# Optimization experiments

Hardware: AMD Instinct MI355X
Metric: run time of the kernel (lower is better)

## Reference

```python
import jax, jax.numpy as jnp
import numpy as np

B, L, D = 2, 2048, 1024
NUM_HEADS = 16
HEAD_DIM = D // NUM_HEADS


def setup_inputs() -> dict:
    key = jax.random.key(0)
    k1, k2 = jax.random.split(key)
    x = jax.random.normal(k1, (B, L, D), dtype=jnp.float32)
    # torch Linear(input_dim, 3*output_dim, bias=False); store as [in, 3*out] for x @ W
    W_qkv = jax.random.normal(k2, (D, 3 * D), dtype=jnp.float32) * (1.0 / np.sqrt(D))
    return {"x": x, "W_qkv": W_qkv}


def reference(x, W_qkv):
    b, l, d = x.shape
    h, hd = NUM_HEADS, HEAD_DIM
    qkv = x @ W_qkv                                  # [B, L, 3*D]
    qkv = qkv.reshape(b, l, 3, h, hd)
    q = jnp.transpose(qkv[:, :, 0], (0, 2, 1, 3))    # [B, H, L, hd]
    k = jnp.transpose(qkv[:, :, 1], (0, 2, 1, 3))
    v = jnp.transpose(qkv[:, :, 2], (0, 2, 1, 3))
    scale = 1.0 / jnp.sqrt(jnp.asarray(hd, dtype=x.dtype))
    scores = jnp.einsum('bhqd,bhkd->bhqk', q, k) * scale   # [B, H, L, L]
    causal = jnp.triu(jnp.ones((l, l), dtype=bool), k=1)   # True above diagonal -> masked
    scores = jnp.where(causal, -jnp.inf, scores)
    attn = jax.nn.softmax(scores, axis=-1)
    # dropout p=0.0 -> identity (eval mode)
    out = jnp.einsum('bhqk,bhkd->bhqd', attn, v)            # [B, H, L, hd]
    out = jnp.transpose(out, (0, 2, 1, 3)).reshape(b, l, h * hd)
    return out
```

## Files before the change

### kernel.cpp

```cpp
#include <hip/hip_runtime.h>
#include <hip/hip_bf16.h>
#include <math.h>

#define NB_L 2048
#define GM 4096
#define GN 3072
#define GK 1024
#define NROWS 65536
#define SCALE_L2E 0.180336880f

typedef float  f4v __attribute__((ext_vector_type(4)));
typedef short  s4v __attribute__((ext_vector_type(4)));
typedef short  s8v __attribute__((ext_vector_type(8)));

#define MFMA_16x16x32(a, b, c) __builtin_amdgcn_mfma_f32_16x16x32_bf16((a), (b), (c), 0, 0, 0)
#define MFMA_16x16x16(a, b, c) __builtin_amdgcn_mfma_f32_16x16x16bf16_1k((a), (b), (c), 0, 0, 0)

static __device__ __forceinline__ unsigned int bfpk(float a, float b) {
    __hip_bfloat162 h = __float22bfloat162_rn(float2{a, b});
    union { __hip_bfloat162 h2; unsigned int u; } cv; cv.h2 = h; return cv.u;
}
static __device__ __forceinline__ unsigned int pkrnd(float a, float b) {
    union { float f; unsigned int u; } ua, ub;
    ua.f = a; ub.f = b;
    return __builtin_amdgcn_perm(ub.u + 0x8000u, ua.u + 0x8000u, 0x07060302u);
}
static __device__ __forceinline__ unsigned short bf1(float a) {
    union { __hip_bfloat16 h; unsigned short u; } cv; cv.h = __float2bfloat16(a); return cv.u;
}
static __device__ __forceinline__ float bf2f(unsigned short u) {
    union { unsigned int u; float f; } cv; cv.u = ((unsigned int)u) << 16; return cv.f;
}

static __device__ __forceinline__ void gl_lds16(const ushort* g, ushort* l) {
    __builtin_amdgcn_global_load_lds((const __attribute__((address_space(1))) void*)g,
                                     (__attribute__((address_space(3))) void*)l, 16, 0, 0);
}

__global__ __launch_bounds__(256) void conv_fused(
    const float* __restrict__ X, const float* __restrict__ W,
    ushort* __restrict__ Xb, ushort* __restrict__ Wt)
{
    __shared__ __align__(16) ushort T[64][72];
    const int bid = blockIdx.x, t = threadIdx.x;
    if (bid < 2048) {
        const int i = bid * 256 + t;
        const float4 f0 = ((const float4*)X)[2 * i];
        const float4 f1 = ((const float4*)X)[2 * i + 1];
        uint4 u;
        u.x = bfpk(f0.x, f0.y); u.y = bfpk(f0.z, f0.w);
        u.z = bfpk(f1.x, f1.y); u.w = bfpk(f1.z, f1.w);
        ((uint4*)Xb)[i] = u;
    } else {
        const int wb = bid - 2048;
        const int k0 = (wb & 15) * 64, n0 = (wb >> 4) * 64;
        {
            const int kr = t >> 2, nc0 = (t & 3) * 16;
            const float* src = W + (size_t)(k0 + kr) * GN + n0 + nc0;
#pragma unroll
            for (int u = 0; u < 4; ++u) {
                const float4 v = *(const float4*)(src + 4 * u);
                T[nc0 + 4 * u + 0][kr] = bf1(v.x);
                T[nc0 + 4 * u + 1][kr] = bf1(v.y);
                T[nc0 + 4 * u + 2][kr] = bf1(v.z);
                T[nc0 + 4 * u + 3][kr] = bf1(v.w);
            }
        }
        __syncthreads();
        {
            const int nr = t >> 2, kc0 = (t & 3) * 16;
            ushort* dst = Wt + (size_t)(n0 + nr) * GK + k0 + kc0;
            *(s8v*)dst       = *(const s8v*)&T[nr][kc0];
            *(s8v*)(dst + 8) = *(const s8v*)&T[nr][kc0 + 8];
        }
    }
}

__global__ __launch_bounds__(512, 2) void qkv_gemm_bf16(
    const ushort* __restrict__ Xb, const ushort* __restrict__ Wt,
    ushort* __restrict__ Qh, ushort* __restrict__ Kh, ushort* __restrict__ VT)
{
    __shared__ __align__(16) ushort As[2][2][128][32];
    __shared__ __align__(16) ushort Bs[2][2][384][32];

    const int tid = threadIdx.x;
    const int bid = blockIdx.x;

    const int xcd = bid & 7, idx = bid >> 3;
    const int ytile = ((xcd >> 1) << 3) + (idx & 7);
    const int xtile = ((xcd & 1) << 2) + (idx >> 3);
    const int row0 = ytile << 7;
    const int col0 = xtile * 384;

    const int lane = tid & 63, w = tid >> 6;
    const int wm = w >> 2, wn = w & 3;
    const int lq = lane & 15, quad = lane >> 4;

    const int rS = tid >> 2, pA = tid & 3;
    const int cA = pA ^ ((rS >> 1) & 3);
    const ushort* gA0 = Xb + (size_t)(row0 + rS) * GK + cA * 8;
    const ushort* gB0 = Wt + (size_t)(col0 + rS) * GK + cA * 8;

    const int pq = (quad ^ ((lq >> 1) & 3)) * 8;
    const int rowA = wm * 64 + lq;
    const int rowB = wn * 96 + lq;

    f4v acc[4][6];
#pragma unroll
    for (int mf = 0; mf < 4; ++mf)
#pragma unroll
        for (int nf = 0; nf < 6; ++nf) acc[mf][nf] = 0.f;

    auto stA = [&](int t, int h) {
        gl_lds16(gA0 + t * 64 + h * 32, &As[t & 1][h][rS][pA * 8]);
    };
    auto stB = [&](int t, int h, int u) {
        gl_lds16(gB0 + (size_t)u * 128 * GK + t * 64 + h * 32,
                 &Bs[t & 1][h][u * 128 + rS][pA * 8]);
    };

    stA(0, 0);
    stB(0, 0, 0); stB(0, 0, 1); stB(0, 0, 2);
    stA(0, 1);
    stB(0, 1, 0); stB(0, 1, 1); stB(0, 1, 2);
    stA(1, 0);
    stB(1, 0, 0); stB(1, 0, 1); stB(1, 0, 2);
    asm volatile("s_waitcnt vmcnt(4)" ::: "memory");
    __builtin_amdgcn_s_barrier();
    asm volatile("" ::: "memory");

    const int NT = GK / 64;
#pragma unroll 2
    for (int t = 0; t < NT; ++t) {
        const int cur = t & 1;
        s8v af[4], bfr[3];

#pragma unroll
        for (int nf = 0; nf < 3; ++nf) bfr[nf] = *(const s8v*)&Bs[cur][0][rowB + nf * 16][pq];
#pragma unroll
        for (int mf = 0; mf < 4; ++mf) af[mf] = *(const s8v*)&As[cur][0][rowA + mf * 16][pq];
        if (t + 1 < NT) { stB(t + 1, 1, 0); stB(t + 1, 1, 1); stB(t + 1, 1, 2); }
        __builtin_amdgcn_s_barrier();
        asm volatile("s_waitcnt lgkmcnt(0)");
        __builtin_amdgcn_s_setprio(1);
#pragma unroll
        for (int mf = 0; mf < 4; ++mf)
#pragma unroll
            for (int nf = 0; nf < 3; ++nf)
                acc[mf][nf] = MFMA_16x16x32(af[mf], bfr[nf], acc[mf][nf]);
        __builtin_amdgcn_s_setprio(0);
        __builtin_amdgcn_s_barrier();

#pragma unroll
        for (int nf = 0; nf < 3; ++nf) bfr[nf] = *(const s8v*)&Bs[cur][0][rowB + 48 + nf * 16][pq];
        if (t + 1 < NT) stA(t + 1, 1);
        __builtin_amdgcn_s_barrier();
        asm volatile("s_waitcnt lgkmcnt(0)");
        __builtin_amdgcn_s_setprio(1);
#pragma unroll
        for (int mf = 0; mf < 4; ++mf)
#pragma unroll
            for (int nf = 0; nf < 3; ++nf)
                acc[mf][nf + 3] = MFMA_16x16x32(af[mf], bfr[nf], acc[mf][nf + 3]);
        __builtin_amdgcn_s_setprio(0);
        __builtin_amdgcn_s_barrier();

#pragma unroll
        for (int nf = 0; nf < 3; ++nf) bfr[nf] = *(const s8v*)&Bs[cur][1][rowB + nf * 16][pq];
#pragma unroll
        for (int mf = 0; mf < 4; ++mf) af[mf] = *(const s8v*)&As[cur][1][rowA + mf * 16][pq];
        if (t + 2 < NT) stA(t + 2, 0);
        __builtin_amdgcn_s_barrier();
        asm volatile("s_waitcnt lgkmcnt(0)");
        __builtin_amdgcn_s_setprio(1);
#pragma unroll
        for (int mf = 0; mf < 4; ++mf)
#pragma unroll
            for (int nf = 0; nf < 3; ++nf)
                acc[mf][nf] = MFMA_16x16x32(af[mf], bfr[nf], acc[mf][nf]);
        __builtin_amdgcn_s_setprio(0);
        __builtin_amdgcn_s_barrier();

#pragma unroll
        for (int nf = 0; nf < 3; ++nf) bfr[nf] = *(const s8v*)&Bs[cur][1][rowB + 48 + nf * 16][pq];
        if (t + 2 < NT) { stB(t + 2, 0, 0); stB(t + 2, 0, 1); stB(t + 2, 0, 2); }
        __builtin_amdgcn_s_barrier();
        asm volatile("s_waitcnt lgkmcnt(0)");
        __builtin_amdgcn_s_setprio(1);
#pragma unroll
        for (int mf = 0; mf < 4; ++mf)
#pragma unroll
            for (int nf = 0; nf < 3; ++nf)
                acc[mf][nf + 3] = MFMA_16x16x32(af[mf], bfr[nf], acc[mf][nf + 3]);
        __builtin_amdgcn_s_setprio(0);
        if (t + 2 < NT) asm volatile("s_waitcnt vmcnt(4)" ::: "memory");
        else            asm volatile("s_waitcnt vmcnt(0)" ::: "memory");
        __builtin_amdgcn_s_barrier();
        asm volatile("" ::: "memory");
    }

#pragma unroll
    for (int mf = 0; mf < 4; ++mf)
#pragma unroll
        for (int nf = 0; nf < 6; ++nf) {
            const int colg = col0 + wn * 96 + nf * 16 + lq;
            const int part = colg >> 10;
            const int colp = colg & 1023;
            const int hh = colp >> 6, d = colp & 63;
#pragma unroll
            for (int r = 0; r < 4; ++r) {
                const int row = row0 + wm * 64 + mf * 16 + quad * 4 + r;
                const int b = row >> 11, tok = row & 2047;
                const int bh = b * 16 + hh;
                if (part == 0) {
                    Qh[((size_t)bh * 2048 + tok) * 64 + d] = bf1(acc[mf][nf][r] * SCALE_L2E);
                } else if (part == 1) {
                    Kh[((size_t)bh * 2048 + tok) * 64 + (d ^ ((tok & 7) << 3))] = bf1(acc[mf][nf][r]);
                } else {
                    VT[((size_t)bh * 64 + d) * 2048 + (tok ^ ((d & 7) << 3))] = bf1(acc[mf][nf][r]);
                }
            }
        }
}

__global__ __launch_bounds__(512, 4) void attn_bf16(
    const ushort* __restrict__ Qh, const ushort* __restrict__ Kh,
    const ushort* __restrict__ VT, ushort* __restrict__ Opart, float* __restrict__ Lp)
{
    __shared__ __align__(16) ushort Ks[2][64 * 64];
    __shared__ __align__(16) ushort Vt[2][64 * 64];

    const int x = blockIdx.x;
    const int bh = x & 31;
    const int y = x >> 5;
    const int s = y & 1;
    const int qp = y >> 1;

    const int tid = threadIdx.x;
    const int w = tid >> 6, lane = tid & 63;
    const int lq = lane & 15, quad = lane >> 4;
    const int kswz = (lq & 7) << 3;

    const ushort* kbase = Kh + (size_t)bh * 2048 * 64;
    const ushort* vbase = VT + (size_t)bh * 64 * 2048;
    const int kr = tid >> 3, ko = (tid & 7) * 8;

    auto stage = [&](int kt, int bufi) {
        gl_lds16(kbase + (size_t)kt * 64 * 64 + kr * 64 + ko, &Ks[bufi][tid * 8]);
        gl_lds16(vbase + (size_t)kr * 2048 + kt * 64 + ko,    &Vt[bufi][tid * 8]);
    };

    const s4v ones = { (short)0x3F80, (short)0x3F80, (short)0x3F80, (short)0x3F80 };

#pragma unroll 1
    for (int piece = 0; piece < 2; ++piece) {
        const int qt = piece ? (15 - qp) : qp;
        const int qrow_base = qt * 128 + w * 16;
        const int diag = 2 * qt + (w >> 2);
        const int kt_lo = s ? (qt + 1) : 0;
        const int niter = qt + 1;

        if (piece) __builtin_amdgcn_s_barrier();

        s8v qf[2];
#pragma unroll
        for (int sb = 0; sb < 2; ++sb)
            qf[sb] = *(const s8v*)(Qh + ((size_t)bh * 2048 + qrow_base + lq) * 64
                                   + sb * 32 + quad * 8);

        f4v o[4];
#pragma unroll
        for (int dg = 0; dg < 4; ++dg) o[dg] = 0.f;
        f4v lacc = 0.f;

        auto compute = [&](int ktc, int bufi) {
            if (ktc > diag) return;
            f4v st[4];
#pragma unroll
            for (int kg = 0; kg < 4; ++kg) st[kg] = 0.f;
#pragma unroll
            for (int kg = 0; kg < 4; ++kg)
#pragma unroll
                for (int sb = 0; sb < 2; ++sb) {
                    const s8v af = *(const s8v*)&Ks[bufi][(kg * 16 + lq) * 64
                                                         + ((sb * 32 + quad * 8) ^ kswz)];
                    st[kg] = MFMA_16x16x32(af, qf[sb], st[kg]);
                }
            if (ktc == diag) {
                const int qrow = qrow_base + lq;
#pragma unroll
                for (int kg = 0; kg < 4; ++kg)
#pragma unroll
                    for (int r = 0; r < 4; ++r)
                        if (ktc * 64 + kg * 16 + quad * 4 + r > qrow)
                            st[kg][r] = -INFINITY;
            }
#pragma unroll
            for (int kg = 0; kg < 4; ++kg)
#pragma unroll
                for (int r = 0; r < 4; ++r)
                    st[kg][r] = exp2f(st[kg][r]);
#pragma unroll
            for (int ks = 0; ks < 4; ++ks) {
                s4v pb;
                {
                    union { s4v v; uint2 u; } c;
                    c.u.x = pkrnd(st[ks][0], st[ks][1]);
                    c.u.y = pkrnd(st[ks][2], st[ks][3]);
                    pb = c.v;
                }
                lacc = MFMA_16x16x16(ones, pb, lacc);
#pragma unroll
                for (int dg = 0; dg < 4; ++dg) {
                    const s4v va = *(const s4v*)&Vt[bufi][(dg * 16 + lq) * 64
                                                         + ((ks * 16 + quad * 4) ^ kswz)];
                    o[dg] = MFMA_16x16x16(va, pb, o[dg]);
                }
            }
        };

        stage(kt_lo, 0);
#pragma unroll 1
        for (int i = 0; i < niter; ++i) {
            const int cur = i & 1;
            __builtin_amdgcn_s_barrier();
            if (i + 1 < niter) {
                stage(kt_lo + i + 1, cur ^ 1);
                asm volatile("s_waitcnt vmcnt(2)" ::: "memory");
            } else {
                asm volatile("s_waitcnt vmcnt(0)" ::: "memory");
            }
            __builtin_amdgcn_s_barrier();
            compute(kt_lo + i, cur);
        }

        {
            const size_t prow = (size_t)(s * 32 + bh) * 2048 + qrow_base + lq;
#pragma unroll
            for (int dg = 0; dg < 4; ++dg) {
                const int d = dg * 16 + quad * 4;
                uint2 u;
                u.x = bfpk(o[dg][0], o[dg][1]);
                u.y = bfpk(o[dg][2], o[dg][3]);
                *(uint2*)&Opart[prow * 64 + d] = u;
            }
            if (quad == 0) Lp[prow] = lacc[0];
        }
    }
}

__global__ __launch_bounds__(256) void attn_combine(
    const ushort* __restrict__ Opart, const float* __restrict__ Lp, float* __restrict__ Out)
{
    const int id = blockIdx.x * 256 + threadIdx.x;
    const int row = id >> 4, c4 = (id & 15) * 4;
    const float l0 = Lp[row], l1 = Lp[row + NROWS];
    const float inv = 1.0f / (l0 + l1);

    const s4v a = *(const s4v*)&Opart[(size_t)row * 64 + c4];
    const s4v c = *(const s4v*)&Opart[(size_t)(row + NROWS) * 64 + c4];
    float4 v;
    v.x = (bf2f((unsigned short)a[0]) + bf2f((unsigned short)c[0])) * inv;
    v.y = (bf2f((unsigned short)a[1]) + bf2f((unsigned short)c[1])) * inv;
    v.z = (bf2f((unsigned short)a[2]) + bf2f((unsigned short)c[2])) * inv;
    v.w = (bf2f((unsigned short)a[3]) + bf2f((unsigned short)c[3])) * inv;

    const int bh = row >> 11, qrow = row & 2047;
    const int b = bh >> 4, h = bh & 15;
    *(float4*)(Out + ((size_t)(b * 2048 + qrow)) * 1024 + h * 64 + c4) = v;
}

extern "C" void kernel_launch(void* const* d_in, const int* in_sizes, int n_in,
                              void* d_out, int out_size, void* d_ws, size_t ws_size,
                              hipStream_t stream)
{
    const float* x  = (const float*)d_in[0];
    const float* wq = (const float*)d_in[1];
    float* out = (float*)d_out;

    const size_t HEADTEN = (size_t)32 * 2048 * 64;
    ushort* wsp = (ushort*)d_ws;
    ushort* qh = wsp;
    ushort* kh = qh + HEADTEN;
    ushort* vt = kh + HEADTEN;
    ushort* xb = vt + HEADTEN;
    ushort* wt = xb + (size_t)GM * GK;
    ushort* opart = xb;
    float*  lp    = (float*)(opart + (size_t)2 * NROWS * 64);

    conv_fused<<<2816, 256, 0, stream>>>(x, wq, xb, wt);
    qkv_gemm_bf16<<<256, 512, 0, stream>>>(xb, wt, qh, kh, vt);
    attn_bf16<<<512, 512, 0, stream>>>(qh, kh, vt, opart, lp);
    attn_combine<<<NROWS * 16 / 256, 256, 0, stream>>>(opart, lp, out);
}
```

Before: 163.9 us.

## Split causal attention KV range four ways and stage partials in output buffer

The attention kernel now splits each query tile's key range into four chunks instead of two, doubling the grid to 1024 blocks and raising the occupancy hint in launch bounds. The two extra partial outputs are written as packed bf16 pairs into the fp32 output buffer, so no extra workspace is needed. The combine kernel then sums four partial row-sums and four partial outputs before normalizing. This adds parallelism across the GPU, at the cost of more partial-output traffic, scattered 2-byte stores and a read-modify-write in the combine step.

```diff
diff --git a/kernel.cpp b/kernel.cpp
--- a/kernel.cpp
+++ b/kernel.cpp
@@ -223,9 +223,10 @@
         }
 }
 
-__global__ __launch_bounds__(512, 4) void attn_bf16(
+__global__ __launch_bounds__(512, 8) void attn_bf16(
     const ushort* __restrict__ Qh, const ushort* __restrict__ Kh,
-    const ushort* __restrict__ VT, ushort* __restrict__ Opart, float* __restrict__ Lp)
+    const ushort* __restrict__ VT, ushort* __restrict__ Opart,
+    float* __restrict__ Lp, float* __restrict__ OutS)
 {
     __shared__ __align__(16) ushort Ks[2][64 * 64];
     __shared__ __align__(16) ushort Vt[2][64 * 64];
@@ -233,8 +234,8 @@
     const int x = blockIdx.x;
     const int bh = x & 31;
     const int y = x >> 5;
-    const int s = y & 1;
-    const int qp = y >> 1;
+    const int s = y & 3;
+    const int qp = y >> 2;
 
     const int tid = threadIdx.x;
     const int w = tid >> 6, lane = tid & 63;
@@ -257,8 +258,10 @@
         const int qt = piece ? (15 - qp) : qp;
         const int qrow_base = qt * 128 + w * 16;
         const int diag = 2 * qt + (w >> 2);
-        const int kt_lo = s ? (qt + 1) : 0;
-        const int niter = qt + 1;
+        const int T = 2 * qt + 2;
+        const int kt_lo = (s * T) >> 2;
+        const int kt_hi = ((s + 1) * T) >> 2;
+        const int niter = kt_hi - kt_lo;
 
         if (piece) __builtin_amdgcn_s_barrier();
 
@@ -319,30 +322,47 @@
             }
         };
 
-        stage(kt_lo, 0);
+        if (niter > 0) {
+            stage(kt_lo, 0);
 #pragma unroll 1
-        for (int i = 0; i < niter; ++i) {
-            const int cur = i & 1;
-            __builtin_amdgcn_s_barrier();
-            if (i + 1 < niter) {
-                stage(kt_lo + i + 1, cur ^ 1);
-                asm volatile("s_waitcnt vmcnt(2)" ::: "memory");
+            for (int i = 0; i < niter; ++i) {
+                const int cur = i & 1;
+                __builtin_amdgcn_s_barrier();
+                if (i + 1 < niter) {
+                    stage(kt_lo + i + 1, cur ^ 1);
+                    asm volatile("s_waitcnt vmcnt(2)" ::: "memory");
+                } else {
+                    asm volatile("s_waitcnt vmcnt(0)" ::: "memory");
+                }
+                __builtin_amdgcn_s_barrier();
+                compute(kt_lo + i, cur);
+            }
+        }
+
+        {
+            const int qrow = qrow_base + lq;
+            const size_t prow = (size_t)(s * 32 + bh) * 2048 + qrow;
+            if (s < 2) {
+#pragma unroll
+                for (int dg = 0; dg < 4; ++dg) {
+                    const int d = dg * 16 + quad * 4;
+                    uint2 u;
+                    u.x = bfpk(o[dg][0], o[dg][1]);
+                    u.y = bfpk(o[dg][2], o[dg][3]);
+                    *(uint2*)&Opart[prow * 64 + d] = u;
+                }
             } else {
-                asm volatile("s_waitcnt vmcnt(0)" ::: "memory");
-            }
-            __builtin_amdgcn_s_barrier();
-            compute(kt_lo + i, cur);
-        }
-
-        {
-            const size_t prow = (size_t)(s * 32 + bh) * 2048 + qrow_base + lq;
-#pragma unroll
-            for (int dg = 0; dg < 4; ++dg) {
-                const int d = dg * 16 + quad * 4;
-                uint2 u;
-                u.x = bfpk(o[dg][0], o[dg][1]);
-                u.y = bfpk(o[dg][2], o[dg][3]);
-                *(uint2*)&Opart[prow * 64 + d] = u;
+                const int b_ = bh >> 4, h = bh & 15;
+                const size_t fbase = ((size_t)(b_ * 2048 + qrow)) * 1024 + h * 64;
+                ushort* op = (ushort*)OutS;
+                const int hilo = s & 1;
+#pragma unroll
+                for (int dg = 0; dg < 4; ++dg) {
+                    const int d = dg * 16 + quad * 4;
+#pragma unroll
+                    for (int r = 0; r < 4; ++r)
+                        op[2 * (fbase + d + r) + hilo] = bf1(o[dg][r]);
+                }
             }
             if (quad == 0) Lp[prow] = lacc[0];
         }
@@ -354,20 +374,28 @@
 {
     const int id = blockIdx.x * 256 + threadIdx.x;
     const int row = id >> 4, c4 = (id & 15) * 4;
-    const float l0 = Lp[row], l1 = Lp[row + NROWS];
-    const float inv = 1.0f / (l0 + l1);
+    const float l = Lp[row] + Lp[row + NROWS] + Lp[row + 2 * NROWS] + Lp[row + 3 * NROWS];
+    const float inv = 1.0f / l;
 
     const s4v a = *(const s4v*)&Opart[(size_t)row * 64 + c4];
     const s4v c = *(const s4v*)&Opart[(size_t)(row + NROWS) * 64 + c4];
-    float4 v;
-    v.x = (bf2f((unsigned short)a[0]) + bf2f((unsigned short)c[0])) * inv;
-    v.y = (bf2f((unsigned short)a[1]) + bf2f((unsigned short)c[1])) * inv;
-    v.z = (bf2f((unsigned short)a[2]) + bf2f((unsigned short)c[2])) * inv;
-    v.w = (bf2f((unsigned short)a[3]) + bf2f((unsigned short)c[3])) * inv;
 
     const int bh = row >> 11, qrow = row & 2047;
     const int b = bh >> 4, h = bh & 15;
-    *(float4*)(Out + ((size_t)(b * 2048 + qrow)) * 1024 + h * 64 + c4) = v;
+    float* outp = Out + ((size_t)(b * 2048 + qrow)) * 1024 + h * 64 + c4;
+    const uint4 slot = *(const uint4*)outp;
+
+    float4 v;
+    v.x = (bf2f((unsigned short)a[0]) + bf2f((unsigned short)c[0])
+         + bf2f((unsigned short)(slot.x & 0xffff)) + bf2f((unsigned short)(slot.x >> 16))) * inv;
+    v.y = (bf2f((unsigned short)a[1]) + bf2f((unsigned short)c[1])
+         + bf2f((unsigned short)(slot.y & 0xffff)) + bf2f((unsigned short)(slot.y >> 16))) * inv;
+    v.z = (bf2f((unsigned short)a[2]) + bf2f((unsigned short)c[2])
+         + bf2f((unsigned short)(slot.z & 0xffff)) + bf2f((unsigned short)(slot.z >> 16))) * inv;
+    v.w = (bf2f((unsigned short)a[3]) + bf2f((unsigned short)c[3])
+         + bf2f((unsigned short)(slot.w & 0xffff)) + bf2f((unsigned short)(slot.w >> 16))) * inv;
+
+    *(float4*)outp = v;
 }
 
 extern "C" void kernel_launch(void* const* d_in, const int* in_sizes, int n_in,
@@ -390,6 +418,6 @@
 
     conv_fused<<<2816, 256, 0, stream>>>(x, wq, xb, wt);
     qkv_gemm_bf16<<<256, 512, 0, stream>>>(xb, wt, qh, kh, vt);
-    attn_bf16<<<512, 512, 0, stream>>>(qh, kh, vt, opart, lp);
+    attn_bf16<<<1024, 512, 0, stream>>>(qh, kh, vt, opart, lp, out);
     attn_combine<<<NROWS * 16 / 256, 256, 0, stream>>>(opart, lp, out);
 }
```

After: 211.0 us. 1.29x slower.
